# Kernel optimization log

Measured on AMD Instinct MI355X. Metric: run time of the kernel, lower is better.

The kernel has to match this reference:

```python
import jax, jax.numpy as jnp
import numpy as np

N_MEL = 80
PRENET = 256
ENC = 512
ARNN = 1024
DRNN = 1024
ATT = 128
NF = 32
K = 31
B, S, T = 16, 256, 400


def _lstm_cell(x, h, c, Wih, Whh, bih, bhh):
    # torch nn.LSTMCell math: gates ordered i, f, g, o
    z = x @ Wih.T + bih + h @ Whh.T + bhh
    i, f, g, o = jnp.split(z, 4, axis=-1)
    c_new = jax.nn.sigmoid(f) * c + jax.nn.sigmoid(i) * jnp.tanh(g)
    h_new = jax.nn.sigmoid(o) * jnp.tanh(c_new)
    return h_new, c_new


def setup_inputs() -> dict:
    key = jax.random.key(0)
    ks = jax.random.split(key, 24)
    g = lambda i, shape: (jax.random.normal(ks[i], shape, jnp.float32) * 0.02)
    inp = {
        'memory': jax.random.normal(ks[0], (B, S, ENC), jnp.float32),
        'decoder_inputs': jax.random.normal(ks[1], (B, N_MEL, T), jnp.float32),
        # prenet (LinearNorm, no bias in tacotron2 prenet)
        'Wpre1': g(2, (PRENET, N_MEL)),
        'Wpre2': g(3, (PRENET, PRENET)),
        # attention LSTMCell: input = prenet + enc = 256 + 512 = 768
        'Wih_a': g(4, (4 * ARNN, PRENET + ENC)),
        'Whh_a': g(5, (4 * ARNN, ARNN)),
        'bih_a': jnp.zeros((4 * ARNN,), jnp.float32),
        'bhh_a': jnp.zeros((4 * ARNN,), jnp.float32),
        # location-sensitive attention
        'Wq': g(6, (ATT, ARNN)),
        'Wm': g(7, (ATT, ENC)),
        'v': g(8, (ATT,)),
        'Wloc_conv': g(9, (NF, 2, K)),
        'Wloc_dense': g(10, (ATT, NF)),
        # decoder LSTMCell: input = att_rnn + enc = 1024 + 512 = 1536
        'Wih_d': g(11, (4 * DRNN, ARNN + ENC)),
        'Whh_d': g(12, (4 * DRNN, DRNN)),
        'bih_d': jnp.zeros((4 * DRNN,), jnp.float32),
        'bhh_d': jnp.zeros((4 * DRNN,), jnp.float32),
        # projections from [decoder_hidden ; context] = 1536
        'Wproj': g(13, (N_MEL, DRNN + ENC)),
        'bproj': jnp.zeros((N_MEL,), jnp.float32),
        'Wgate': g(14, (1, DRNN + ENC)),
        'bgate': jnp.zeros((1,), jnp.float32),
        'memory_lengths': jax.random.randint(ks[15], (B,), S // 2, S + 1),
    }
    return inp


def reference(memory, decoder_inputs, Wpre1, Wpre2, Wih_a, Whh_a, bih_a, bhh_a,
              Wq, Wm, v, Wloc_conv, Wloc_dense, Wih_d, Whh_d, bih_d, bhh_d,
              Wproj, bproj, Wgate, bgate, memory_lengths):
    # pad mask: True where position is beyond the encoder length
    pad_mask = jnp.arange(S)[None, :] >= memory_lengths[:, None]  # [B,S]
    proc_mem = memory @ Wm.T  # [B,S,ATT], memory_layer precomputed once

    # parse_decoder_inputs + go frame: [B,80,T] -> [T,B,80], prepend zeros
    di = jnp.transpose(decoder_inputs, (2, 0, 1))
    di = jnp.concatenate([jnp.zeros((1, B, N_MEL), di.dtype), di], axis=0)
    # prenet (dropout treated as identity for deterministic reference)
    pre = jax.nn.relu(jax.nn.relu(di @ Wpre1.T) @ Wpre2.T)  # [T+1,B,256]
    xs = pre[:-1]  # loop consumes indices 0..T-1

    carry0 = (jnp.zeros((B, ARNN)), jnp.zeros((B, ARNN)),
              jnp.zeros((B, DRNN)), jnp.zeros((B, DRNN)),
              jnp.zeros((B, S)), jnp.zeros((B, S)), jnp.zeros((B, ENC)))

    def step(carry, x):
        ah, ac, dh, dc, aw, awc, ctx = carry
        ah, ac = _lstm_cell(jnp.concatenate([x, ctx], -1), ah, ac,
                            Wih_a, Whh_a, bih_a, bhh_a)
        # location features from [prev_weights ; cum_weights]
        awcat = jnp.stack([aw, awc], axis=1)  # [B,2,S]
        loc = jax.lax.conv_general_dilated(
            awcat, Wloc_conv, (1,), ((K // 2, K // 2),),
            dimension_numbers=('NCH', 'OIH', 'NCH'))  # [B,NF,S]
        proc_att = jnp.einsum('bfs,af->bsa', loc, Wloc_dense)  # [B,S,ATT]
        q = ah @ Wq.T  # [B,ATT]
        e = jnp.tanh(q[:, None, :] + proc_att + proc_mem) @ v  # [B,S]
        e = jnp.where(pad_mask, -1e9, e)
        aw = jax.nn.softmax(e, axis=-1)
        ctx = jnp.einsum('bs,bse->be', aw, memory)  # [B,ENC]
        awc = awc + aw
        dh, dc = _lstm_cell(jnp.concatenate([ah, ctx], -1), dh, dc,
                            Wih_d, Whh_d, bih_d, bhh_d)
        hac = jnp.concatenate([dh, ctx], -1)  # [B,1536]
        mel = hac @ Wproj.T + bproj  # [B,80]
        gate = (hac @ Wgate.T + bgate)[:, 0]  # [B]
        return (ah, ac, dh, dc, aw, awc, ctx), (mel, gate, aw)

    _, (mels, gates, aligns) = jax.lax.scan(step, carry0, xs)
    mel_outputs = jnp.transpose(mels, (1, 2, 0))  # [B,80,T]
    gate_outputs = gates.T  # [B,T]
    alignments = jnp.transpose(aligns, (1, 0, 2))  # [B,T,S]
    return mel_outputs, gate_outputs, alignments
```

## Files before the change

### kernel.cpp

```cpp
#include <hip/hip_runtime.h>

typedef unsigned short ushort_t;
typedef unsigned int uint_t;
typedef float f32x4_t __attribute__((ext_vector_type(4)));
typedef short bf16x8_t __attribute__((ext_vector_type(8)));

#define NBATCH 16
#define SMEM   256
#define TSTEPS 400

#define F_XSB   0u
#define F_PM    819200u
#define F_MMIX  1343488u
#define F_W1T   1675264u
#define F_W2T   1695744u
#define F_AHB   1761280u
#define F_DHB   1777664u
#define F_CTXB  1794048u
#define F_DHF   1802240u
#define F_AWG   1835008u
#define F_FLG   1851392u
#define ZERO_BASE  F_AHB
#define ZERO_COUNT 95616u
#define F_QP    1856896u

#define AHF  0
#define CTXF 64
#define DHFL 192
#define AWF  320
#define PRF  336

#define A_AH    0
#define A_CTX   32768
#define A_XS    49152
#define A_RED   57344
#define A_QWQ   61440
#define A_QH    69632
#define D_AH    0
#define D_CTX   32768
#define D_DH    49152
#define D_COMB  81920
#define T_LOCU  0
#define T_QSM   20480
#define T_VSM   20992
#define T_ESM   21504
#define T_RED   22528
#define T_SMAW  22784
#define T_SMAWC 23808
#define T_QRED  24832
#define C_MEM   0
#define C_PART  131072
#define C_AWS   135168
#define P_DHP   0
#define P_AWP   65536
#define SMEM_BYTES 136192

struct Ptrs {
  const float *memory, *dec_in, *Wpre1, *Wpre2, *Wih_a, *Whh_a, *bih_a, *bhh_a,
              *Wq, *Wm, *v, *Wc, *Wld, *Wih_d, *Whh_d, *bih_d, *bhh_d,
              *Wproj, *bproj, *Wgate, *bgate;
  const int *mlen;
  float *ws;
  float *out;
};

__device__ __forceinline__ float ftanh(float x) {
  float e = __expf(2.f * x);
  return 1.f - 2.f / (e + 1.f);
}
__device__ __forceinline__ float fsig(float x) { return 1.f / (1.f + __expf(-x)); }

__device__ __forceinline__ unsigned f2bfbits(float x) {
  unsigned u = __builtin_bit_cast(unsigned, x);
  return (u + 0x7FFFu + ((u >> 16) & 1u)) >> 16;
}
__device__ __forceinline__ float bf2f(ushort_t u) {
  unsigned v = ((unsigned)u) << 16;
  return __builtin_bit_cast(float, v);
}
__device__ __forceinline__ bf16x8_t packbf8(const float* f) {
  bf16x8_t r;
#pragma unroll
  for (int j = 0; j < 8; ++j) r[j] = (short)f2bfbits(f[j]);
  return r;
}
__device__ __forceinline__ bf16x8_t pack_from_f4(const float* src) {
  const float4* s4 = (const float4*)src;
  float4 lo = s4[0], hi = s4[1];
  float tmp[8] = {lo.x, lo.y, lo.z, lo.w, hi.x, hi.y, hi.z, hi.w};
  return packbf8(tmp);
}
__device__ __forceinline__ bf16x8_t ldbf8(const ushort_t* p) {
  return *(const bf16x8_t*)p;
}
__device__ __forceinline__ unsigned long long ldull_a(const unsigned long long* p) {
  return __hip_atomic_load(p, __ATOMIC_RELAXED, __HIP_MEMORY_SCOPE_AGENT);
}
__device__ __forceinline__ void stull_a(unsigned long long* p, unsigned long long v) {
  __hip_atomic_store(p, v, __ATOMIC_RELAXED, __HIP_MEMORY_SCOPE_AGENT);
}
__device__ __forceinline__ void stf_a(float* p, float v) {
  __hip_atomic_store(p, v, __ATOMIC_RELAXED, __HIP_MEMORY_SCOPE_AGENT);
}
__device__ __forceinline__ float ldf_a(const float* p) {
  return __hip_atomic_load(p, __ATOMIC_RELAXED, __HIP_MEMORY_SCOPE_AGENT);
}
__device__ __forceinline__ void pollge(int* flg, int slot, int thr) {
  while (__hip_atomic_load(flg + slot * 16, __ATOMIC_RELAXED, __HIP_MEMORY_SCOPE_AGENT) < thr)
    __builtin_amdgcn_s_sleep(1);
}
__device__ __forceinline__ void sig(int* flg, int slot, int val) {
  __hip_atomic_store(flg + slot * 16, val, __ATOMIC_RELAXED, __HIP_MEMORY_SCOPE_AGENT);
}
__device__ __forceinline__ void lds_st8(char* smc, int base, int row, int row_sh,
                                        int bytecol, unsigned long long v) {
  *(unsigned long long*)(smc + base + (row << row_sh) + (bytecol ^ ((row & 7) << 4))) = v;
}
__device__ __forceinline__ bf16x8_t lds_bf8(const char* smc, int base, int row,
                                            int row_sh, int bytecol) {
  return *(const bf16x8_t*)(smc + base + (row << row_sh) + (bytecol ^ ((row & 7) << 4)));
}
#define MFMA16(a,b,c) __builtin_amdgcn_mfma_f32_16x16x32_bf16((a),(b),(c),0,0,0)

__global__ __launch_bounds__(256) void k_zero(Ptrs p) {
  unsigned i = blockIdx.x * 256 + threadIdx.x;
  if (i < ZERO_COUNT) p.ws[ZERO_BASE + i] = 0.f;
}

__global__ __launch_bounds__(256) void k_transpose(Ptrs p) {
  int i = blockIdx.x * 256 + threadIdx.x;
  if (i < 20480) {
    int m = i >> 8, c = i & 255;
    p.ws[F_W1T + i] = p.Wpre1[c * 80 + m];
  } else if (i < 20480 + 65536) {
    int j = i - 20480;
    int pp = j >> 8, q = j & 255;
    p.ws[F_W2T + j] = p.Wpre2[q * 256 + pp];
  }
}

__global__ __launch_bounds__(256) void k_prenet(Ptrs p) {
  __shared__ float dil[NBATCH * 80];
  __shared__ float h1[NBATCH * 256];
  const int t = blockIdx.x, tid = threadIdx.x;
  const float* W1T = p.ws + F_W1T;
  const float* W2T = p.ws + F_W2T;

  for (int i = tid; i < NBATCH * 80; i += 256) {
    int b = i / 80, m = i - b * 80;
    dil[i] = (t == 0) ? 0.f : p.dec_in[((size_t)b * 80 + m) * 400 + (t - 1)];
  }
  __syncthreads();

  float acc[NBATCH];
#pragma unroll
  for (int b = 0; b < NBATCH; ++b) acc[b] = 0.f;
  for (int m = 0; m < 80; ++m) {
    float w = W1T[m * 256 + tid];
#pragma unroll
    for (int b = 0; b < NBATCH; ++b) acc[b] = fmaf(dil[b * 80 + m], w, acc[b]);
  }
#pragma unroll
  for (int b = 0; b < NBATCH; ++b) h1[b * 256 + tid] = fmaxf(acc[b], 0.f);
  __syncthreads();

#pragma unroll
  for (int b = 0; b < NBATCH; ++b) acc[b] = 0.f;
  for (int q = 0; q < 256; ++q) {
    float w = W2T[q * 256 + tid];
#pragma unroll
    for (int b = 0; b < NBATCH; ++b) acc[b] = fmaf(h1[b * 256 + q], w, acc[b]);
  }
  ushort_t* xsbU = (ushort_t*)(p.ws + F_XSB);
#pragma unroll
  for (int b = 0; b < NBATCH; ++b)
    xsbU[((size_t)(t * NBATCH + b)) * 256 + tid] = (ushort_t)f2bfbits(fmaxf(acc[b], 0.f));
}

__global__ __launch_bounds__(256) void k_procmem(Ptrs p) {
  __shared__ alignas(16) float msl[16 * 512];
  const int b = blockIdx.x >> 4, s0 = (blockIdx.x & 15) << 4;
  const int tid = threadIdx.x;
  const float4* src = (const float4*)(p.memory + ((size_t)(b * SMEM + s0)) * 512);
  float4* dst = (float4*)msl;
  for (int i = tid; i < 16 * 512 / 4; i += 256) dst[i] = src[i];
  __syncthreads();

  const int a = tid & 127, sg = tid >> 7;
  const float4* wm = (const float4*)(p.Wm + (size_t)a * 512);
  float* pm = p.ws + F_PM;
  float acc[8];
#pragma unroll
  for (int j = 0; j < 8; ++j) acc[j] = 0.f;
  for (int k = 0; k < 128; ++k) {
    float4 w = wm[k];
#pragma unroll
    for (int j = 0; j < 8; ++j) {
      float4 m = ((const float4*)(msl + (size_t)(sg * 8 + j) * 512))[k];
      acc[j] += w.x * m.x + w.y * m.y + w.z * m.z + w.w * m.w;
    }
  }
#pragma unroll
  for (int j = 0; j < 8; ++j)
    pm[((size_t)(b * SMEM + s0 + sg * 8 + j)) * 128 + a] = acc[j];
}

__global__ __launch_bounds__(512) void k_premix(Ptrs p) {
  const int b = blockIdx.x, tid = threadIdx.x;
  float* M = p.ws + F_MMIX;
  for (int i = tid; i < 81 * 256; i += 512) {
    int row = i >> 8, s = i & 255;
    const float* wrow = (row < 80) ? p.Wproj + (size_t)row * 1536 + 1024 : p.Wgate + 1024;
    const float4* w4 = (const float4*)wrow;
    const float4* m4 = (const float4*)(p.memory + ((size_t)(b * 256 + s)) * 512);
    float acc = 0.f;
#pragma unroll 4
    for (int k = 0; k < 128; ++k) {
      float4 w = w4[k], m = m4[k];
      acc += w.x * m.x + w.y * m.y + w.z * m.z + w.w * m.w;
    }
    M[((size_t)b * 81 + row) * 256 + s] = acc;
  }
}

__global__ __launch_bounds__(512, 1) void k_scan(Ptrs p) {
  extern __shared__ char smc[];
  const int bid = blockIdx.x, tid = threadIdx.x;
  const int wid = tid >> 6, lane = tid & 63;
  const int m16 = lane & 15, kq = lane >> 4;

  float* ws = p.ws;
  ushort_t* xsbU  = (ushort_t*)(ws + F_XSB);
  float*    pmF   = ws + F_PM;
  float*    Mx    = ws + F_MMIX;
  unsigned long long* ahb8 = (unsigned long long*)(ws + F_AHB);
  unsigned long long* dhb8 = (unsigned long long*)(ws + F_DHB);
  unsigned long long* ctxb8 = (unsigned long long*)(ws + F_CTXB);
  float*    dhfF  = ws + F_DHF;
  float*    awGF  = ws + F_AWG;
  float*    qpF   = ws + F_QP;
  int*      flg   = (int*)(ws + F_FLG);
  float* out_mel  = p.out;
  float* out_gate = p.out + 512000;
  float* out_al   = p.out + 518400;

  if (bid < 64) {
    const int ls = wid >> 1, half = wid & 1;
    const int strip = (bid << 2) | ls;
    const int gA = m16 & 3, jA = m16 >> 2;
    const int wrowA = gA * 1024 + strip * 4 + jA;
    bf16x8_t wA[28];
#pragma unroll
    for (int c = 0; c < 28; ++c) {
      int k0 = (half * 28 + c) * 32 + kq * 8;
      const float* src = (k0 < 768) ? p.Wih_a + (size_t)wrowA * 768 + k0
                                    : p.Whh_a + (size_t)wrowA * 1024 + (k0 - 768);
      wA[c] = pack_from_f4(src);
    }
    const int nnA = strip * 4 + kq;
    float biasA[4];
#pragma unroll
    for (int r = 0; r < 4; ++r) biasA[r] = p.bih_a[r * 1024 + nnA] + p.bhh_a[r * 1024 + nnA];
    float acState = 0.f;
    float* ared = (float*)(smc + A_RED);
    float* qwq  = (float*)(smc + A_QWQ);
    float* qh   = (float*)(smc + A_QH);
    for (int i = tid; i < 2048; i += 512) {
      int a = i >> 4, c = i & 15;
      qwq[i] = p.Wq[(size_t)a * 1024 + bid * 16 + c];
    }
    __syncthreads();

    for (int t = 0; t < TSTEPS; ++t) {
      const int pc = t & 1, pp = (t + 1) & 1;
      if (tid < 64) pollge(flg, AHF + tid, t);
      else if (tid >= 96 && tid < 224) pollge(flg, DHFL + (tid - 96), t - 1);
      __syncthreads();
      {
        const unsigned long long* ag = ahb8 + (size_t)pp * 4096;
        const unsigned long long* xg = (const unsigned long long*)xsbU + (size_t)t * 1024;
        unsigned long long tA[8], tX[2];
#pragma unroll
        for (int i = 0; i < 8; ++i) tA[i] = ldull_a(ag + tid + i * 512);
#pragma unroll
        for (int i = 0; i < 2; ++i) tX[i] = xg[tid + i * 512];
#pragma unroll
        for (int i = 0; i < 8; ++i) { int u = tid + i * 512; lds_st8(smc, A_AH, u >> 8, 11, (u & 255) * 8, tA[i]); }
#pragma unroll
        for (int i = 0; i < 2; ++i) { int u = tid + i * 512; lds_st8(smc, A_XS, u >> 6, 9, (u & 63) * 8, tX[i]); }
      }
      if (tid >= 64 && tid < 96) pollge(flg, CTXF + (tid - 64), t);
      __syncthreads();
      {
        const unsigned long long* cg = ctxb8 + (size_t)pp * 2048;
        unsigned long long tC[4];
#pragma unroll
        for (int i = 0; i < 4; ++i) tC[i] = ldull_a(cg + tid + i * 512);
#pragma unroll
        for (int i = 0; i < 4; ++i) { int u = tid + i * 512; lds_st8(smc, A_CTX, u >> 7, 10, (u & 127) * 8, tC[i]); }
      }
      __syncthreads();

      f32x4_t a0 = {0,0,0,0}, a1 = {0,0,0,0};
      if (half == 0) {
#pragma unroll
        for (int c = 0; c < 28; ++c) {
          bf16x8_t bf;
          if (c < 8)       bf = lds_bf8(smc, A_XS,  m16, 9,  c * 64 + kq * 16);
          else if (c < 24) bf = lds_bf8(smc, A_CTX, m16, 10, (c - 8) * 64 + kq * 16);
          else             bf = lds_bf8(smc, A_AH,  m16, 11, (c - 24) * 64 + kq * 16);
          if (c & 1) a1 = MFMA16(wA[c], bf, a1); else a0 = MFMA16(wA[c], bf, a0);
        }
      } else {
#pragma unroll
        for (int c = 0; c < 28; ++c) {
          bf16x8_t bf = lds_bf8(smc, A_AH, m16, 11, (4 + c) * 64 + kq * 16);
          if (c & 1) a1 = MFMA16(wA[c], bf, a1); else a0 = MFMA16(wA[c], bf, a0);
        }
#pragma unroll
        for (int r = 0; r < 4; ++r) ared[((ls * 64 + lane) << 2) + r] = a0[r] + a1[r];
      }
      __syncthreads();
      if (half == 0) {
        float z[4];
#pragma unroll
        for (int r = 0; r < 4; ++r)
          z[r] = a0[r] + a1[r] + ared[((ls * 64 + lane) << 2) + r] + biasA[r];
        float cn = fsig(z[1]) * acState + fsig(z[0]) * ftanh(z[2]);
        acState = cn;
        float h = fsig(z[3]) * ftanh(cn);
        qh[(m16 << 4) + ls * 4 + kq] = h;
        unsigned hb = f2bfbits(h);
        unsigned b0 = __shfl(hb, m16);
        unsigned b1 = __shfl(hb, m16 + 16);
        unsigned b2 = __shfl(hb, m16 + 32);
        unsigned b3 = __shfl(hb, m16 + 48);
        if (kq == 0) {
          unsigned long long u = (unsigned long long)(b0 | (b1 << 16))
                               | ((unsigned long long)(b2 | (b3 << 16)) << 32);
          stull_a(ahb8 + ((size_t)(pc * 16 + m16)) * 256 + strip, u);
        }
      }
      __syncthreads();
      {
        int a = tid & 127, bg = tid >> 7;
        const float* wrow = qwq + a * 16;
        float s0 = 0.f, s1 = 0.f, s2 = 0.f, s3 = 0.f;
#pragma unroll
        for (int c = 0; c < 16; ++c) {
          float wv = wrow[c];
          s0 = fmaf(wv, qh[((bg * 4 + 0) << 4) + c], s0);
          s1 = fmaf(wv, qh[((bg * 4 + 1) << 4) + c], s1);
          s2 = fmaf(wv, qh[((bg * 4 + 2) << 4) + c], s2);
          s3 = fmaf(wv, qh[((bg * 4 + 3) << 4) + c], s3);
        }
        float* qps = qpF + (size_t)pc * 131072 + bid * 2048 + a;
        stf_a(qps + (size_t)(bg * 4 + 0) * 128, s0);
        stf_a(qps + (size_t)(bg * 4 + 1) * 128, s1);
        stf_a(qps + (size_t)(bg * 4 + 2) * 128, s2);
        stf_a(qps + (size_t)(bg * 4 + 3) * 128, s3);
      }
      __syncthreads();
      if (tid == 0) sig(flg, AHF + bid, t + 1);
    }
  } else if (bid < 192) {
    const int ls = wid >> 2, qt = wid & 3;
    const int strip = ((bid - 64) << 1) | ls;
    const int gD = m16 & 3, jD = m16 >> 2;
    const int wrowD = gD * 1024 + strip * 4 + jD;
    bf16x8_t wD[20];
#pragma unroll
    for (int c = 0; c < 20; ++c) {
      int k0 = (qt * 20 + c) * 32 + kq * 8;
      const float* src = (k0 < 1536) ? p.Wih_d + (size_t)wrowD * 1536 + k0
                                     : p.Whh_d + (size_t)wrowD * 1024 + (k0 - 1536);
      wD[c] = pack_from_f4(src);
    }
    const int nnD = strip * 4 + kq;
    float biasD[4];
#pragma unroll
    for (int r = 0; r < 4; ++r) biasD[r] = p.bih_d[r * 1024 + nnD] + p.bhh_d[r * 1024 + nnD];
    float dcState = 0.f;
    float* comb = (float*)(smc + D_COMB);
    __syncthreads();

    for (int t = 1; t <= TSTEPS; ++t) {
      const int pc = t & 1, pw = (t + 1) & 1;
      if (tid < 64) pollge(flg, AHF + tid, t);
      else if (tid >= 96 && tid < 224) pollge(flg, DHFL + (tid - 96), t - 1);
      else if (tid >= 224 && tid < 232) pollge(flg, PRF + (tid - 224), t - 2);
      __syncthreads();
      {
        const unsigned long long* ag = ahb8 + (size_t)pw * 4096;
        const unsigned long long* dg = dhb8 + (size_t)pc * 4096;
        unsigned long long tA[8], tD[8];
#pragma unroll
        for (int i = 0; i < 8; ++i) tA[i] = ldull_a(ag + tid + i * 512);
#pragma unroll
        for (int i = 0; i < 8; ++i) tD[i] = ldull_a(dg + tid + i * 512);
#pragma unroll
        for (int i = 0; i < 8; ++i) { int u = tid + i * 512; lds_st8(smc, D_AH, u >> 8, 11, (u & 255) * 8, tA[i]); }
#pragma unroll
        for (int i = 0; i < 8; ++i) { int u = tid + i * 512; lds_st8(smc, D_DH, u >> 8, 11, (u & 255) * 8, tD[i]); }
      }
      if (tid >= 64 && tid < 96) pollge(flg, CTXF + (tid - 64), t);
      __syncthreads();
      {
        const unsigned long long* cg = ctxb8 + (size_t)pw * 2048;
        unsigned long long tC[4];
#pragma unroll
        for (int i = 0; i < 4; ++i) tC[i] = ldull_a(cg + tid + i * 512);
#pragma unroll
        for (int i = 0; i < 4; ++i) { int u = tid + i * 512; lds_st8(smc, D_CTX, u >> 7, 10, (u & 127) * 8, tC[i]); }
      }
      __syncthreads();

      f32x4_t a0 = {0,0,0,0}, a1 = {0,0,0,0};
#define DFRAG_AH(ch)  lds_bf8(smc, D_AH,  m16, 11, (ch) * 64 + kq * 16)
#define DFRAG_CTX(ch) lds_bf8(smc, D_CTX, m16, 10, (ch) * 64 + kq * 16)
#define DFRAG_DH(ch)  lds_bf8(smc, D_DH,  m16, 11, (ch) * 64 + kq * 16)
#define DMFMA(BF) { bf16x8_t bf = (BF); \
        if (c & 1) a1 = MFMA16(wD[c], bf, a1); else a0 = MFMA16(wD[c], bf, a0); }
      if (qt == 0) {
#pragma unroll
        for (int c = 0; c < 20; ++c) DMFMA(DFRAG_AH(c))
      } else if (qt == 1) {
#pragma unroll
        for (int c = 0; c < 20; ++c) { if (c < 12) DMFMA(DFRAG_AH(20 + c)) else DMFMA(DFRAG_CTX(c - 12)) }
      } else if (qt == 2) {
#pragma unroll
        for (int c = 0; c < 20; ++c) { if (c < 8) DMFMA(DFRAG_CTX(8 + c)) else DMFMA(DFRAG_DH(c - 8)) }
      } else {
#pragma unroll
        for (int c = 0; c < 20; ++c) DMFMA(DFRAG_DH(12 + c))
      }
#undef DMFMA
      if (qt != 0) {
#pragma unroll
        for (int r = 0; r < 4; ++r)
          comb[(((ls * 3 + qt - 1) * 64 + lane) << 2) + r] = a0[r] + a1[r];
      }
      __syncthreads();
      if (qt == 0) {
        float z[4];
#pragma unroll
        for (int r = 0; r < 4; ++r) {
          z[r] = a0[r] + a1[r] + biasD[r];
#pragma unroll
          for (int j = 0; j < 3; ++j) z[r] += comb[(((ls * 3 + j) * 64 + lane) << 2) + r];
        }
        float cn = fsig(z[1]) * dcState + fsig(z[0]) * ftanh(z[2]);
        dcState = cn;
        float h = fsig(z[3]) * ftanh(cn);
        stf_a(dhfF + (size_t)pw * 16384 + m16 * 1024 + nnD, h);
        unsigned hb = f2bfbits(h);
        unsigned b0 = __shfl(hb, m16);
        unsigned b1 = __shfl(hb, m16 + 16);
        unsigned b2 = __shfl(hb, m16 + 32);
        unsigned b3 = __shfl(hb, m16 + 48);
        if (kq == 0) {
          unsigned long long u = (unsigned long long)(b0 | (b1 << 16))
                               | ((unsigned long long)(b2 | (b3 << 16)) << 32);
          stull_a(dhb8 + ((size_t)(pw * 16 + m16)) * 256 + strip, u);
        }
      }
      __syncthreads();
      if (tid == 0) sig(flg, DHFL + (bid - 64), t);
    }
  } else if (bid < 208) {
    const int b = bid - 192;
    const int mlenb = p.mlen[b];
    ushort_t* locu = (ushort_t*)(smc + T_LOCU);
    float* qsm   = (float*)(smc + T_QSM);
    float* vsm   = (float*)(smc + T_VSM);
    float* esm   = (float*)(smc + T_ESM);
    float* red   = (float*)(smc + T_RED);
    float* smaw  = (float*)(smc + T_SMAW);
    float* smawc = (float*)(smc + T_SMAWC);
    float* qred  = (float*)(smc + T_QRED);

    bf16x8_t wLd[8];
#pragma unroll
    for (int at = 0; at < 8; ++at)
      wLd[at] = pack_from_f4(p.Wld + ((size_t)(at * 16 + m16)) * 32 + kq * 8);
    bf16x8_t wC[2][2];
#pragma unroll
    for (int ft = 0; ft < 2; ++ft)
#pragma unroll
      for (int ck = 0; ck < 2; ++ck) {
        float tmp[8];
#pragma unroll
        for (int jj = 0; jj < 8; ++jj) {
          int k2 = ck * 32 + kq * 8 + jj;
          float vv = 0.f;
          if (k2 < 62) { int ch = (k2 < 31) ? 0 : 1; int k = k2 - 31 * ch;
            vv = p.Wc[((size_t)(ft * 16 + m16) * 2 + ch) * 31 + k]; }
          tmp[jj] = vv;
        }
        wC[ft][ck] = packbf8(tmp);
      }
    uint_t pmreg[2][8][2];
#pragma unroll
    for (int u = 0; u < 2; ++u) {
      int sloc = (wid * 2 + u) * 16 + m16;
#pragma unroll
      for (int at = 0; at < 8; ++at)
#pragma unroll
        for (int rp = 0; rp < 2; ++rp) {
          const float* src = pmF + ((size_t)(b * 256 + sloc)) * 128 + at * 16 + kq * 4 + rp * 2;
          pmreg[u][at][rp] = f2bfbits(src[0]) | (f2bfbits(src[1]) << 16);
        }
    }
    if (tid < 128) vsm[tid] = p.v[tid];
    if (tid < 256) { smaw[tid] = 0.f; smawc[tid] = 0.f; }
    __syncthreads();

    for (int t = 0; t < TSTEPS; ++t) {
#pragma unroll
      for (int u = 0; u < 4; ++u) {
        int task = wid * 4 + u;
        int stile = task >> 1, ft = task & 1;
        int scol = stile * 16 + m16;
        f32x4_t acc = {0,0,0,0};
#pragma unroll
        for (int ck = 0; ck < 2; ++ck) {
          float tmp[8];
#pragma unroll
          for (int jj = 0; jj < 8; ++jj) {
            int k2 = ck * 32 + kq * 8 + jj;
            float vv = 0.f;
            if (k2 < 62) {
              int ch = (k2 < 31) ? 0 : 1; int k = k2 - 31 * ch;
              int sp = scol + k - 15;
              if (sp >= 0 && sp < 256) vv = (ch ? smawc : smaw)[sp];
            }
            tmp[jj] = vv;
          }
          acc = MFMA16(wC[ft][ck], packbf8(tmp), acc);
        }
#pragma unroll
        for (int r = 0; r < 4; ++r)
          locu[scol * 40 + ft * 16 + kq * 4 + r] = (ushort_t)f2bfbits(acc[r]);
      }
      if (tid < 64) pollge(flg, AHF + tid, t + 1);
      else if (tid < 72) pollge(flg, PRF + (tid - 64), t - 3);
      __syncthreads();
      {
        int a = tid & 127, g = tid >> 7;
        const float* qps = qpF + (size_t)(t & 1) * 131072 + b * 128 + a;
        float s = 0.f;
#pragma unroll
        for (int k = 0; k < 16; ++k)
          s += ldf_a(qps + (size_t)(g * 16 + k) * 2048);
        qred[g * 128 + a] = s;
      }
      __syncthreads();
      if (tid < 128) qsm[tid] = qred[tid] + qred[128 + tid] + qred[256 + tid] + qred[384 + tid];
      __syncthreads();
#pragma unroll
      for (int u = 0; u < 2; ++u) {
        int sloc = (wid * 2 + u) * 16 + m16;
        bf16x8_t Bfrag = ldbf8(locu + sloc * 40 + kq * 8);
        float eacc = 0.f;
#pragma unroll
        for (int at = 0; at < 8; ++at) {
          f32x4_t C = {0,0,0,0};
          C = MFMA16(wLd[at], Bfrag, C);
#pragma unroll
          for (int r = 0; r < 4; ++r) {
            int a = at * 16 + kq * 4 + r;
            uint_t pw_ = pmreg[u][at][r >> 1];
            float pmv = bf2f((ushort_t)((r & 1) ? (pw_ >> 16) : (pw_ & 0xFFFF)));
            eacc = fmaf(vsm[a], ftanh(C[r] + qsm[a] + pmv), eacc);
          }
        }
        eacc += __shfl_xor(eacc, 16);
        eacc += __shfl_xor(eacc, 32);
        if (sloc >= mlenb) eacc = -1.0e9f;
        if (kq == 0) esm[sloc] = eacc;
      }
      __syncthreads();
      float ev = 0.f;
      if (tid < 256) {
        ev = esm[tid];
        float mv = ev;
        for (int o = 32; o; o >>= 1) mv = fmaxf(mv, __shfl_xor(mv, o));
        if (lane == 0) red[wid] = mv;
      }
      __syncthreads();
      float gmax = fmaxf(fmaxf(red[0], red[1]), fmaxf(red[2], red[3]));
      float pv = 0.f;
      if (tid < 256) {
        pv = __expf(ev - gmax);
        float sv = pv;
        for (int o = 32; o; o >>= 1) sv += __shfl_xor(sv, o);
        if (lane == 0) red[8 + wid] = sv;
      }
      __syncthreads();
      float gsum = red[8] + red[9] + red[10] + red[11];
      float awv = 0.f;
      if (tid < 256) {
        awv = pv / gsum;
        smaw[tid] = awv;
        smawc[tid] += awv;
        stf_a(awGF + (size_t)(t & 3) * 4096 + b * 256 + tid, awv);
      }
      __syncthreads();
      if (tid == 0) sig(flg, AWF + b, t + 1);
      if (tid < 256) out_al[((size_t)b * 400 + t) * 256 + tid] = awv;
    }
  } else if (bid < 216) {
    const int wv = (bid - 208) * 8 + wid;
    int rows[2] = {wv * 2, wv * 2 + 1};
    float wdh[2][16], mreg[2][16][4], biasr[2];
#pragma unroll
    for (int rr = 0; rr < 2; ++rr) {
      int row = rows[rr];
      biasr[rr] = 0.f;
#pragma unroll
      for (int j = 0; j < 16; ++j) wdh[rr][j] = 0.f;
#pragma unroll
      for (int b2 = 0; b2 < 16; ++b2)
#pragma unroll
        for (int j = 0; j < 4; ++j) mreg[rr][b2][j] = 0.f;
      if (row <= 80) {
        const float* wsrc = (row < 80) ? p.Wproj + (size_t)row * 1536 : p.Wgate;
#pragma unroll
        for (int j = 0; j < 16; ++j) wdh[rr][j] = wsrc[lane + 64 * j];
        biasr[rr] = (row < 80) ? p.bproj[row] : p.bgate[0];
#pragma unroll
        for (int b2 = 0; b2 < 16; ++b2)
#pragma unroll
          for (int j = 0; j < 4; ++j)
            mreg[rr][b2][j] = Mx[((size_t)b2 * 81 + row) * 256 + lane + 64 * j];
      }
    }
    float* dhp = (float*)(smc + P_DHP);
    float* awp = (float*)(smc + P_AWP);
    __syncthreads();
    for (int t = 1; t <= TSTEPS; ++t) {
      const int pw = (t + 1) & 1;
      if (tid < 128) pollge(flg, DHFL + tid, t);
      else if (tid < 144) pollge(flg, AWF + tid - 128, t);
      __syncthreads();
      {
        const unsigned long long* ag = (const unsigned long long*)(awGF + (size_t)((t - 1) & 3) * 4096);
        const unsigned long long* dg = (const unsigned long long*)(dhfF + (size_t)pw * 16384);
        unsigned long long tw[4], td[16];
#pragma unroll
        for (int i = 0; i < 4; ++i) tw[i] = ldull_a(ag + tid + i * 512);
#pragma unroll
        for (int i = 0; i < 16; ++i) td[i] = ldull_a(dg + tid + i * 512);
#pragma unroll
        for (int i = 0; i < 4; ++i) ((unsigned long long*)awp)[tid + i * 512] = tw[i];
#pragma unroll
        for (int i = 0; i < 16; ++i) ((unsigned long long*)dhp)[tid + i * 512] = td[i];
      }
      __syncthreads();
      if (wv <= 40) {
        for (int b2 = 0; b2 < 16; ++b2) {
          float h[16];
#pragma unroll
          for (int j = 0; j < 16; ++j) h[j] = dhp[b2 * 1024 + lane + 64 * j];
#pragma unroll
          for (int rr = 0; rr < 2; ++rr) {
            if (rows[rr] > 80) continue;
            float d = 0.f;
#pragma unroll
            for (int j = 0; j < 16; ++j) d = fmaf(wdh[rr][j], h[j], d);
#pragma unroll
            for (int j = 0; j < 4; ++j) d = fmaf(mreg[rr][b2][j], awp[b2 * 256 + lane + 64 * j], d);
            for (int o = 32; o; o >>= 1) d += __shfl_xor(d, o);
            if (lane == 0) {
              d += biasr[rr];
              if (rows[rr] < 80) out_mel[((size_t)b2 * 80 + rows[rr]) * 400 + (t - 1)] = d;
              else out_gate[(size_t)b2 * 400 + (t - 1)] = d;
            }
          }
        }
      }
      __syncthreads();
      if (tid == 0) sig(flg, PRF + (bid - 208), t);
    }
  } else if (bid < 248) {
    const int cbid = bid - 216;
    const int b = cbid >> 1, half2 = cbid & 1;
    ushort_t* memu2 = (ushort_t*)(smc + C_MEM);
    float* part = (float*)(smc + C_PART);
    float* awsm = (float*)(smc + C_AWS);
    for (int i = tid; i < 16384; i += 512) {
      int s = i >> 6, c4 = i & 63;
      float4 m = *(const float4*)(p.memory + ((size_t)(b * 256 + s)) * 512 + half2 * 256 + c4 * 4);
      ushort_t* dst = memu2 + s * 256 + c4 * 4;
      dst[0] = (ushort_t)f2bfbits(m.x);
      dst[1] = (ushort_t)f2bfbits(m.y);
      dst[2] = (ushort_t)f2bfbits(m.z);
      dst[3] = (ushort_t)f2bfbits(m.w);
    }
    __syncthreads();

    for (int t = 0; t < TSTEPS; ++t) {
      const int pc = t & 1;
      if (tid < 64) pollge(flg, AHF + tid, t);
      else if (tid < 192) pollge(flg, DHFL + (tid - 64), t - 1);
      else if (tid == 192) pollge(flg, AWF + b, t + 1);
      __syncthreads();
      if (tid < 256) awsm[tid] = ldf_a(awGF + (size_t)(t & 3) * 4096 + b * 256 + tid);
      __syncthreads();
      const int c = tid & 127, sg = tid >> 7;
      const uint_t* mrow = (const uint_t*)memu2;
      float a0 = 0.f, a1 = 0.f;
#pragma unroll 8
      for (int si = 0; si < 64; ++si) {
        int s = sg * 64 + si;
        uint_t mm = mrow[s * 128 + c];
        float av = awsm[s];
        a0 = fmaf(bf2f((ushort_t)(mm & 0xFFFF)), av, a0);
        a1 = fmaf(bf2f((ushort_t)(mm >> 16)), av, a1);
      }
      part[sg * 256 + c * 2] = a0;
      part[sg * 256 + c * 2 + 1] = a1;
      __syncthreads();
      if (tid < 64) {
        unsigned pk[4];
#pragma unroll
        for (int j = 0; j < 4; ++j) {
          int col = tid * 4 + j;
          float v = part[col] + part[256 + col] + part[512 + col] + part[768 + col];
          pk[j] = f2bfbits(v);
        }
        unsigned long long u = (unsigned long long)(pk[0] | (pk[1] << 16))
                             | ((unsigned long long)(pk[2] | (pk[3] << 16)) << 32);
        stull_a(ctxb8 + ((size_t)(pc * 16 + b)) * 128 + half2 * 64 + tid, u);
      }
      __syncthreads();
      if (tid == 0) sig(flg, CTXF + cbid, t + 1);
    }
  }
}

extern "C" void kernel_launch(void* const* d_in, const int* in_sizes, int n_in,
                              void* d_out, int out_size, void* d_ws, size_t ws_size,
                              hipStream_t stream) {
  (void)in_sizes; (void)n_in; (void)out_size; (void)ws_size;
  Ptrs p;
  p.memory = (const float*)d_in[0];
  p.dec_in = (const float*)d_in[1];
  p.Wpre1  = (const float*)d_in[2];
  p.Wpre2  = (const float*)d_in[3];
  p.Wih_a  = (const float*)d_in[4];
  p.Whh_a  = (const float*)d_in[5];
  p.bih_a  = (const float*)d_in[6];
  p.bhh_a  = (const float*)d_in[7];
  p.Wq     = (const float*)d_in[8];
  p.Wm     = (const float*)d_in[9];
  p.v      = (const float*)d_in[10];
  p.Wc     = (const float*)d_in[11];
  p.Wld    = (const float*)d_in[12];
  p.Wih_d  = (const float*)d_in[13];
  p.Whh_d  = (const float*)d_in[14];
  p.bih_d  = (const float*)d_in[15];
  p.bhh_d  = (const float*)d_in[16];
  p.Wproj  = (const float*)d_in[17];
  p.bproj  = (const float*)d_in[18];
  p.Wgate  = (const float*)d_in[19];
  p.bgate  = (const float*)d_in[20];
  p.mlen   = (const int*)d_in[21];
  p.ws  = (float*)d_ws;
  p.out = (float*)d_out;

  static bool attr_done = false;
  if (!attr_done) {
    hipFuncSetAttribute((const void*)k_scan,
                        hipFuncAttributeMaxDynamicSharedMemorySize, SMEM_BYTES);
    attr_done = true;
  }

  hipLaunchKernelGGL(k_zero,      dim3((ZERO_COUNT + 255) / 256), dim3(256), 0, stream, p);
  hipLaunchKernelGGL(k_transpose, dim3(336), dim3(256), 0, stream, p);
  hipLaunchKernelGGL(k_prenet,    dim3(400), dim3(256), 0, stream, p);
  hipLaunchKernelGGL(k_procmem,   dim3(256), dim3(256), 0, stream, p);
  hipLaunchKernelGGL(k_premix,    dim3(16),  dim3(512), 0, stream, p);
  hipLaunchKernelGGL(k_scan,      dim3(256), dim3(512), SMEM_BYTES, stream, p);
}
```

Baseline: 8.617 ms.

## Fuse context computation into attention blocks and overlap ctx-independent LSTM MFMAs

```diff
diff --git a/kernel.cpp b/kernel.cpp
--- a/kernel.cpp
+++ b/kernel.cpp
@@ -40,20 +40,18 @@
 #define D_CTX   32768
 #define D_DH    49152
 #define D_COMB  81920
-#define T_LOCU  0
-#define T_QSM   20480
-#define T_VSM   20992
-#define T_ESM   21504
-#define T_RED   22528
-#define T_SMAW  22784
-#define T_SMAWC 23808
-#define T_QRED  24832
-#define C_MEM   0
-#define C_PART  131072
-#define C_AWS   135168
+#define M_LOCU  0
+#define M_QSM   20480
+#define M_VSM   20992
+#define M_ESM   21504
+#define M_RED   22528
+#define M_SMAW  22784
+#define M_SMAWC 23808
+#define M_MEM   24832
+#define M_PART  155904
 #define P_DHP   0
 #define P_AWP   65536
-#define SMEM_BYTES 136192
+#define SMEM_BYTES 160000
 
 struct Ptrs {
   const float *memory, *dec_in, *Wpre1, *Wpre2, *Wih_a, *Whh_a, *bih_a, *bhh_a,
@@ -289,7 +287,29 @@
 #pragma unroll
         for (int i = 0; i < 2; ++i) { int u = tid + i * 512; lds_st8(smc, A_XS, u >> 6, 9, (u & 63) * 8, tX[i]); }
       }
-      if (tid >= 64 && tid < 96) pollge(flg, CTXF + (tid - 64), t);
+      __syncthreads();
+      f32x4_t a0 = {0,0,0,0}, a1 = {0,0,0,0};
+      if (half == 0) {
+#pragma unroll
+        for (int c = 0; c < 8; ++c) {
+          bf16x8_t bf = lds_bf8(smc, A_XS, m16, 9, c * 64 + kq * 16);
+          if (c & 1) a1 = MFMA16(wA[c], bf, a1); else a0 = MFMA16(wA[c], bf, a0);
+        }
+#pragma unroll
+        for (int c = 24; c < 28; ++c) {
+          bf16x8_t bf = lds_bf8(smc, A_AH, m16, 11, (c - 24) * 64 + kq * 16);
+          if (c & 1) a1 = MFMA16(wA[c], bf, a1); else a0 = MFMA16(wA[c], bf, a0);
+        }
+      } else {
+#pragma unroll
+        for (int c = 0; c < 28; ++c) {
+          bf16x8_t bf = lds_bf8(smc, A_AH, m16, 11, (4 + c) * 64 + kq * 16);
+          if (c & 1) a1 = MFMA16(wA[c], bf, a1); else a0 = MFMA16(wA[c], bf, a0);
+        }
+#pragma unroll
+        for (int r = 0; r < 4; ++r) ared[((ls * 64 + lane) << 2) + r] = a0[r] + a1[r];
+      }
+      if (tid < 32) pollge(flg, CTXF + tid, t);
       __syncthreads();
       {
         const unsigned long long* cg = ctxb8 + (size_t)pp * 2048;
@@ -300,28 +320,12 @@
         for (int i = 0; i < 4; ++i) { int u = tid + i * 512; lds_st8(smc, A_CTX, u >> 7, 10, (u & 127) * 8, tC[i]); }
       }
       __syncthreads();
-
-      f32x4_t a0 = {0,0,0,0}, a1 = {0,0,0,0};
       if (half == 0) {
 #pragma unroll
-        for (int c = 0; c < 28; ++c) {
-          bf16x8_t bf;
-          if (c < 8)       bf = lds_bf8(smc, A_XS,  m16, 9,  c * 64 + kq * 16);
-          else if (c < 24) bf = lds_bf8(smc, A_CTX, m16, 10, (c - 8) * 64 + kq * 16);
-          else             bf = lds_bf8(smc, A_AH,  m16, 11, (c - 24) * 64 + kq * 16);
+        for (int c = 8; c < 24; ++c) {
+          bf16x8_t bf = lds_bf8(smc, A_CTX, m16, 10, (c - 8) * 64 + kq * 16);
           if (c & 1) a1 = MFMA16(wA[c], bf, a1); else a0 = MFMA16(wA[c], bf, a0);
         }
-      } else {
-#pragma unroll
-        for (int c = 0; c < 28; ++c) {
-          bf16x8_t bf = lds_bf8(smc, A_AH, m16, 11, (4 + c) * 64 + kq * 16);
-          if (c & 1) a1 = MFMA16(wA[c], bf, a1); else a0 = MFMA16(wA[c], bf, a0);
-        }
-#pragma unroll
-        for (int r = 0; r < 4; ++r) ared[((ls * 64 + lane) << 2) + r] = a0[r] + a1[r];
-      }
-      __syncthreads();
-      if (half == 0) {
         float z[4];
 #pragma unroll
         for (int r = 0; r < 4; ++r)
@@ -467,17 +471,20 @@
       __syncthreads();
       if (tid == 0) sig(flg, DHFL + (bid - 64), t);
     }
-  } else if (bid < 208) {
-    const int b = bid - 192;
+  } else if (bid < 224) {
+    const int cbid = bid - 192;
+    const int b = cbid >> 1, h2 = cbid & 1;
     const int mlenb = p.mlen[b];
-    ushort_t* locu = (ushort_t*)(smc + T_LOCU);
-    float* qsm   = (float*)(smc + T_QSM);
-    float* vsm   = (float*)(smc + T_VSM);
-    float* esm   = (float*)(smc + T_ESM);
-    float* red   = (float*)(smc + T_RED);
-    float* smaw  = (float*)(smc + T_SMAW);
-    float* smawc = (float*)(smc + T_SMAWC);
-    float* qred  = (float*)(smc + T_QRED);
+    ushort_t* locu = (ushort_t*)(smc + M_LOCU);
+    float* qsm   = (float*)(smc + M_QSM);
+    float* vsm   = (float*)(smc + M_VSM);
+    float* esm   = (float*)(smc + M_ESM);
+    float* red   = (float*)(smc + M_RED);
+    float* smaw  = (float*)(smc + M_SMAW);
+    float* smawc = (float*)(smc + M_SMAWC);
+    ushort_t* memu2 = (ushort_t*)(smc + M_MEM);
+    float* part  = (float*)(smc + M_PART);
+    float* qred  = part;
 
     bf16x8_t wLd[8];
 #pragma unroll
@@ -511,11 +518,21 @@
           pmreg[u][at][rp] = f2bfbits(src[0]) | (f2bfbits(src[1]) << 16);
         }
     }
+    for (int i = tid; i < 16384; i += 512) {
+      int s = i >> 6, c4 = i & 63;
+      float4 m = *(const float4*)(p.memory + ((size_t)(b * 256 + s)) * 512 + h2 * 256 + c4 * 4);
+      ushort_t* dst = memu2 + s * 256 + c4 * 4;
+      dst[0] = (ushort_t)f2bfbits(m.x);
+      dst[1] = (ushort_t)f2bfbits(m.y);
+      dst[2] = (ushort_t)f2bfbits(m.z);
+      dst[3] = (ushort_t)f2bfbits(m.w);
+    }
     if (tid < 128) vsm[tid] = p.v[tid];
     if (tid < 256) { smaw[tid] = 0.f; smawc[tid] = 0.f; }
     __syncthreads();
 
     for (int t = 0; t < TSTEPS; ++t) {
+      const int pc = t & 1;
 #pragma unroll
       for (int u = 0; u < 4; ++u) {
         int task = wid * 4 + u;
@@ -543,7 +560,8 @@
           locu[scol * 40 + ft * 16 + kq * 4 + r] = (ushort_t)f2bfbits(acc[r]);
       }
       if (tid < 64) pollge(flg, AHF + tid, t + 1);
-      else if (tid < 72) pollge(flg, PRF + (tid - 64), t - 3);
+      else if (tid < 192) pollge(flg, DHFL + (tid - 64), t - 1);
+      else if (tid < 200) pollge(flg, PRF + (tid - 192), t - 3);
       __syncthreads();
       {
         int a = tid & 127, g = tid >> 7;
@@ -603,14 +621,46 @@
         awv = pv / gsum;
         smaw[tid] = awv;
         smawc[tid] += awv;
-        stf_a(awGF + (size_t)(t & 3) * 4096 + b * 256 + tid, awv);
-      }
-      __syncthreads();
-      if (tid == 0) sig(flg, AWF + b, t + 1);
-      if (tid < 256) out_al[((size_t)b * 400 + t) * 256 + tid] = awv;
-    }
-  } else if (bid < 216) {
-    const int wv = (bid - 208) * 8 + wid;
+        if (h2 == 0) stf_a(awGF + (size_t)(t & 3) * 4096 + b * 256 + tid, awv);
+      }
+      __syncthreads();
+      {
+        const int c = tid & 127, sg = tid >> 7;
+        const uint_t* mrow = (const uint_t*)memu2;
+        float c0 = 0.f, c1 = 0.f;
+#pragma unroll 8
+        for (int si = 0; si < 64; ++si) {
+          int s = sg * 64 + si;
+          uint_t mm = mrow[s * 128 + c];
+          float av = smaw[s];
+          c0 = fmaf(bf2f((ushort_t)(mm & 0xFFFF)), av, c0);
+          c1 = fmaf(bf2f((ushort_t)(mm >> 16)), av, c1);
+        }
+        part[sg * 256 + c * 2] = c0;
+        part[sg * 256 + c * 2 + 1] = c1;
+      }
+      __syncthreads();
+      if (tid < 64) {
+        unsigned pk[4];
+#pragma unroll
+        for (int j = 0; j < 4; ++j) {
+          int col = tid * 4 + j;
+          float v = part[col] + part[256 + col] + part[512 + col] + part[768 + col];
+          pk[j] = f2bfbits(v);
+        }
+        unsigned long long u = (unsigned long long)(pk[0] | (pk[1] << 16))
+                             | ((unsigned long long)(pk[2] | (pk[3] << 16)) << 32);
+        stull_a(ctxb8 + ((size_t)(pc * 16 + b)) * 128 + h2 * 64 + tid, u);
+      }
+      __syncthreads();
+      if (tid == 0) {
+        sig(flg, CTXF + cbid, t + 1);
+        if (h2 == 0) sig(flg, AWF + b, t + 1);
+      }
+      if (h2 == 0 && tid < 256) out_al[((size_t)b * 400 + t) * 256 + tid] = awv;
+    }
+  } else if (bid < 232) {
+    const int wv = (bid - 224) * 8 + wid;
     int rows[2] = {wv * 2, wv * 2 + 1};
     float wdh[2][16], mreg[2][16][4], biasr[2];
 #pragma unroll
@@ -680,61 +730,7 @@
         }
       }
       __syncthreads();
-      if (tid == 0) sig(flg, PRF + (bid - 208), t);
-    }
-  } else if (bid < 248) {
-    const int cbid = bid - 216;
-    const int b = cbid >> 1, half2 = cbid & 1;
-    ushort_t* memu2 = (ushort_t*)(smc + C_MEM);
-    float* part = (float*)(smc + C_PART);
-    float* awsm = (float*)(smc + C_AWS);
-    for (int i = tid; i < 16384; i += 512) {
-      int s = i >> 6, c4 = i & 63;
-      float4 m = *(const float4*)(p.memory + ((size_t)(b * 256 + s)) * 512 + half2 * 256 + c4 * 4);
-      ushort_t* dst = memu2 + s * 256 + c4 * 4;
-      dst[0] = (ushort_t)f2bfbits(m.x);
-      dst[1] = (ushort_t)f2bfbits(m.y);
-      dst[2] = (ushort_t)f2bfbits(m.z);
-      dst[3] = (ushort_t)f2bfbits(m.w);
-    }
-    __syncthreads();
-
-    for (int t = 0; t < TSTEPS; ++t) {
-      const int pc = t & 1;
-      if (tid < 64) pollge(flg, AHF + tid, t);
-      else if (tid < 192) pollge(flg, DHFL + (tid - 64), t - 1);
-      else if (tid == 192) pollge(flg, AWF + b, t + 1);
-      __syncthreads();
-      if (tid < 256) awsm[tid] = ldf_a(awGF + (size_t)(t & 3) * 4096 + b * 256 + tid);
-      __syncthreads();
-      const int c = tid & 127, sg = tid >> 7;
-      const uint_t* mrow = (const uint_t*)memu2;
-      float a0 = 0.f, a1 = 0.f;
-#pragma unroll 8
-      for (int si = 0; si < 64; ++si) {
-        int s = sg * 64 + si;
-        uint_t mm = mrow[s * 128 + c];
-        float av = awsm[s];
-        a0 = fmaf(bf2f((ushort_t)(mm & 0xFFFF)), av, a0);
-        a1 = fmaf(bf2f((ushort_t)(mm >> 16)), av, a1);
-      }
-      part[sg * 256 + c * 2] = a0;
-      part[sg * 256 + c * 2 + 1] = a1;
-      __syncthreads();
-      if (tid < 64) {
-        unsigned pk[4];
-#pragma unroll
-        for (int j = 0; j < 4; ++j) {
-          int col = tid * 4 + j;
-          float v = part[col] + part[256 + col] + part[512 + col] + part[768 + col];
-          pk[j] = f2bfbits(v);
-        }
-        unsigned long long u = (unsigned long long)(pk[0] | (pk[1] << 16))
-                             | ((unsigned long long)(pk[2] | (pk[3] << 16)) << 32);
-        stull_a(ctxb8 + ((size_t)(pc * 16 + b)) * 128 + half2 * 64 + tid, u);
-      }
-      __syncthreads();
-      if (tid == 0) sig(flg, CTXF + cbid, t + 1);
+      if (tid == 0) sig(flg, PRF + (bid - 224), t);
     }
   }
 }
@@ -781,5 +777,5 @@
   hipLaunchKernelGGL(k_prenet,    dim3(400), dim3(256), 0, stream, p);
   hipLaunchKernelGGL(k_procmem,   dim3(256), dim3(256), 0, stream, p);
   hipLaunchKernelGGL(k_premix,    dim3(16),  dim3(512), 0, stream, p);
-  hipLaunchKernelGGL(k_scan,      dim3(256), dim3(512), SMEM_BYTES, stream, p);
-}
+  hipLaunchKernelGGL(k_scan,      dim3(232), dim3(512), SMEM_BYTES, stream, p);
+}
```

Result: faster. 8.205 ms (-4.8%).
